# Performance work log

Hardware: AMD Instinct MI355X
Metric: run time of the kernel (lower is better)

Reference implementation:

```python
import jax, jax.numpy as jnp
import numpy as np

N_BINS = 229
OUT_F = 88
MODEL = 128
W_SIZE = 30
WIN = 2 * W_SIZE + 1  # 61


def _window(spec):
    B, T, F = spec.shape
    padded = jnp.pad(spec, ((0, 0), (W_SIZE, W_SIZE), (0, 0)))
    idx = jnp.arange(T)[:, None] + jnp.arange(WIN)[None, :]
    return padded[:, idx, :]


def setup_inputs() -> dict:
    key = jax.random.key(0)
    ks = jax.random.split(key, 12)
    B, T = 4, 1024
    s = 0.05
    return {
        "spec": jax.random.normal(ks[0], (B, T, N_BINS), dtype=jnp.float32),
        # frame_stack: Linear(N_BINS -> OUT_F)
        "W_frame": jax.random.normal(ks[1], (N_BINS, OUT_F), dtype=jnp.float32) * s,
        "b_frame": jnp.zeros((OUT_F,), dtype=jnp.float32),
        # onset attention: Linear(N_BINS + N_BINS -> MODEL), v: Linear(MODEL -> 1, no bias)
        "W_attn_o": jax.random.normal(ks[2], (2 * N_BINS, MODEL), dtype=jnp.float32) * s,
        "b_attn_o": jnp.zeros((MODEL,), dtype=jnp.float32),
        "v_o": jax.random.normal(ks[3], (MODEL,), dtype=jnp.float32) * s,
        # onset linear1: Linear(N_BINS -> OUT_F)
        "W_lin1": jax.random.normal(ks[4], (N_BINS, OUT_F), dtype=jnp.float32) * s,
        "b_lin1": jnp.zeros((OUT_F,), dtype=jnp.float32),
        # combine attention: Linear(2*OUT_F + N_BINS -> MODEL)
        "W_attn_c": jax.random.normal(ks[5], (2 * OUT_F + N_BINS, MODEL), dtype=jnp.float32) * s,
        "b_attn_c": jnp.zeros((MODEL,), dtype=jnp.float32),
        "v_c": jax.random.normal(ks[6], (MODEL,), dtype=jnp.float32) * s,
        # combine linear: Linear(2*OUT_F + N_BINS -> OUT_F)
        "W_linc": jax.random.normal(ks[7], (2 * OUT_F + N_BINS, OUT_F), dtype=jnp.float32) * s,
        "b_linc": jnp.zeros((OUT_F,), dtype=jnp.float32),
    }


def _attend(hidden, win, Wa, ba, v):
    B, T, Wn, F = win.shape
    h = jnp.broadcast_to(hidden[:, :, None, :], (B, T, Wn, hidden.shape[-1]))
    energy = jnp.tanh(jnp.concatenate([h, win], axis=-1) @ Wa + ba)
    scores = energy @ v
    return jax.nn.softmax(scores, axis=-1)


def reference(spec, W_frame, b_frame, W_attn_o, b_attn_o, v_o, W_lin1, b_lin1,
              W_attn_c, b_attn_c, v_c, W_linc, b_linc):
    win = _window(spec)

    feat_pred = spec @ W_frame + b_frame  # [B,T,OUT_F]

    # Onset stack
    a_onset = _attend(spec, win, W_attn_o, b_attn_o, v_o)
    weighted_o = jnp.einsum('btw,btwf->btf', a_onset, win)  # [B,T,N_BINS]
    onset_pred = jax.nn.sigmoid(weighted_o @ W_lin1 + b_lin1)  # [B,T,OUT_F]

    # Combine stack
    x = jnp.concatenate([feat_pred, onset_pred], axis=-1)  # [B,T,2*OUT_F]
    a_frame = _attend(x, win, W_attn_c, b_attn_c, v_c)
    weighted_c = jnp.einsum('btw,btwf->btf', a_frame, win)  # [B,T,N_BINS]
    frame_pred = jax.nn.sigmoid(jnp.concatenate([x, weighted_c], axis=-1) @ W_linc + b_linc)

    return (frame_pred, a_frame[:, :, None, :], onset_pred, a_onset[:, :, None, :], feat_pred)
```

## Files before the change

### kernel.cpp

```cpp
#include <hip/hip_runtime.h>

#define NBINS 229
#define OUTF  88
#define MODEL 128
#define WSZ   30
#define WIN   61
#define TLEN  1024
#define BT    4096

#define NC1 648
#define NP1 704
#define KP1 256
#define NC2 216
#define KP2 192

typedef short bf16x8 __attribute__((ext_vector_type(8)));
typedef float f32x4 __attribute__((ext_vector_type(4)));
typedef unsigned short ushort_t;

__device__ __forceinline__ float sigmoid_f(float x) {
    return __builtin_amdgcn_rcpf(1.f + __expf(-x));
}
__device__ __forceinline__ ushort_t f2bf(float f) {
    unsigned u = __float_as_uint(f);
    return (ushort_t)((u + 0x7fffu + ((u >> 16) & 1u)) >> 16);
}

#define PREP_BLOCKS 2181

__global__ __launch_bounds__(256) void prep_kernel(
    const float* __restrict__ Wf,  const float* __restrict__ bfr,
    const float* __restrict__ Wao, const float* __restrict__ bao,
    const float* __restrict__ Wl1,
    const float* __restrict__ Wac, const float* __restrict__ bac,
    const float* __restrict__ Wlc,
    const float* __restrict__ spec,
    const float* __restrict__ vo, const float* __restrict__ vc,
    ushort_t* __restrict__ B1b, ushort_t* __restrict__ B2b,
    ushort_t* __restrict__ specB, ushort_t* __restrict__ xB,
    float* __restrict__ bias1, float* __restrict__ bias2,
    float* __restrict__ sv)
{
    __shared__ float red[4];
    const int b = blockIdx.x;
    if (b < 704) {
        int idx = b * 256 + threadIdx.x;
        int n = idx >> 8, k = idx & 255;
        float v = 0.f;
        if (k < NBINS && n < NC1) {
            if (n < 88)       v = Wf[k * 88 + n];
            else if (n < 216) v = Wao[k * MODEL + (n - 88)];
            else if (n < 344) v = Wao[(k + NBINS) * MODEL + (n - 216)];
            else if (n < 472) v = Wac[(k + 176) * MODEL + (n - 344)];
            else if (n < 560) v = Wl1[k * 88 + (n - 472)];
            else              v = Wlc[(k + 176) * 88 + (n - 560)];
        }
        B1b[idx] = f2bf(v);
    } else if (b < 896) {
        int idx = (b - 704) * 256 + threadIdx.x;
        int n = idx / 192, k = idx - n * 192;
        float v = 0.f;
        if (k < 176 && n < NC2)
            v = (n < 128) ? Wac[k * MODEL + n] : Wlc[k * 88 + (n - 128)];
        B2b[idx] = f2bf(v);
    } else if (b < 1920) {
        int idx = (b - 896) * 256 + threadIdx.x;
        int r = idx >> 6, k4 = (idx & 63) * 4;
        const float* sp = spec + (size_t)r * NBINS;
        ushort4 o;
        o.x = (k4 + 0 < NBINS) ? f2bf(sp[k4 + 0]) : (ushort_t)0;
        o.y = (k4 + 1 < NBINS) ? f2bf(sp[k4 + 1]) : (ushort_t)0;
        o.z = (k4 + 2 < NBINS) ? f2bf(sp[k4 + 2]) : (ushort_t)0;
        o.w = (k4 + 3 < NBINS) ? f2bf(sp[k4 + 3]) : (ushort_t)0;
        *(ushort4*)&specB[(size_t)r * 256 + k4] = o;
    } else if (b < 2176) {
        int idx = (b - 1920) * 256 + threadIdx.x;
        int r = idx >> 4, c = 176 + (idx & 15);
        xB[(size_t)r * 192 + c] = 0;
    } else if (b < 2180) {
        int idx = (b - 2176) * 256 + threadIdx.x;
        if (idx < 704)
            bias1[idx] = (idx < 88) ? bfr[idx] : (idx < 216 ? bao[idx - 88] : 0.f);
        else if (idx < 960) {
            int n = idx - 704;
            bias2[n] = (n < 128) ? bac[n] : 0.f;
        }
    } else {
        int wid = threadIdx.x >> 6, lane = threadIdx.x & 63;
        const float* vp = (wid < 2) ? vo : vc;
        float val = vp[(wid & 1) * 64 + lane];
#pragma unroll
        for (int m = 32; m; m >>= 1) val += __shfl_xor(val, m, 64);
        if (lane == 0) red[wid] = val;
        __syncthreads();
        if (threadIdx.x == 0) {
            sv[0] = red[0] + red[1];
            sv[1] = red[2] + red[3];
        }
    }
}

template<int KITER, int RTS, int MODE>
__global__ __launch_bounds__(256) void gemm_mfma(
    const ushort_t* __restrict__ Ab, int lka,
    const ushort_t* __restrict__ Bb,
    const float* __restrict__ bias, int Nc,
    float* __restrict__ f0, ushort_t* __restrict__ u0,
    float* __restrict__ f1, ushort_t* __restrict__ u1,
    ushort_t* __restrict__ u2, ushort_t* __restrict__ u3,
    ushort_t* __restrict__ u4)
{
    const int tid = threadIdx.x;
    const int wv = tid >> 6, ln = tid & 63;
    const int l15 = ln & 15, qd = ln >> 4;
    const int flat = blockIdx.y * gridDim.x + blockIdx.x;
    const int e = flat & 7, kf = flat >> 3;
    const int rb = (e * (1 << RTS) + (kf & ((1 << RTS) - 1))) * 64;
    const int cb = (kf >> RTS) * 64;
    const int lkb = KITER * 32;

    const ushort_t* ap = Ab + (size_t)(rb + wv * 16 + l15) * lka + qd * 8;
    const ushort_t* bp[4];
#pragma unroll
    for (int nt = 0; nt < 4; nt++)
        bp[nt] = Bb + (size_t)(cb + nt * 16 + l15) * lkb + qd * 8;

    f32x4 acc[4];
#pragma unroll
    for (int nt = 0; nt < 4; nt++) acc[nt] = (f32x4){0.f, 0.f, 0.f, 0.f};

    bf16x8 af = *(const bf16x8*)ap, bfv[4];
#pragma unroll
    for (int nt = 0; nt < 4; nt++) bfv[nt] = *(const bf16x8*)bp[nt];

    for (int it = 0; it < KITER; it++) {
        bf16x8 an, bn[4];
        const int nk = (it + 1 < KITER) ? (it + 1) * 32 : 0;
        an = *(const bf16x8*)(ap + nk);
#pragma unroll
        for (int nt = 0; nt < 4; nt++) bn[nt] = *(const bf16x8*)(bp[nt] + nk);
#pragma unroll
        for (int nt = 0; nt < 4; nt++)
            acc[nt] = __builtin_amdgcn_mfma_f32_16x16x32_bf16(
                af, bfv[nt], acc[nt], 0, 0, 0);
        af = an;
#pragma unroll
        for (int nt = 0; nt < 4; nt++) bfv[nt] = bn[nt];
    }

    const int mbase = rb + wv * 16 + qd * 4;
#pragma unroll
    for (int nt = 0; nt < 4; nt++) {
        const int n = cb + nt * 16 + l15;
        if (n < Nc) {
            const float bn = bias[n];
#pragma unroll
            for (int r = 0; r < 4; r++) {
                const int m = mbase + r;
                float val = acc[nt][r] + bn;
                if (MODE == 0) {
                    if (n < 88) {
                        f0[(size_t)m * 88 + n] = val;
                        u0[(size_t)m * 192 + n] = f2bf(val);
                    } else if (n < 216) {
                        f1[(size_t)m * 128 + (n - 88)] = __expf(val + val);
                    } else if (n < 344) {
                        u1[(size_t)m * 128 + (n - 216)] = f2bf(__expf(val + val));
                    } else if (n < 472) {
                        u2[(size_t)m * 128 + (n - 344)] = f2bf(__expf(val + val));
                    } else if (n < 560) {
                        u3[(size_t)m * 96 + (n - 472)] = f2bf(val);
                    } else {
                        u4[(size_t)m * 96 + (n - 560)] = f2bf(val);
                    }
                } else {
                    f0[(size_t)m * 216 + n] = (n < 128) ? __expf(val + val) : val;
                }
            }
        }
    }
}

#define EPST 136
#define RST  96

__global__ __launch_bounds__(512) void attn_v8(
    const float* __restrict__ EH_all, int hs,
    const ushort_t* __restrict__ EPb,
    const ushort_t* __restrict__ Rb,
    const float* __restrict__ vvec, const float* __restrict__ svp,
    const float* __restrict__ pred_bias,
    const float* __restrict__ base, int bs,
    float* __restrict__ a_out, float* __restrict__ pred_out,
    ushort_t* __restrict__ xb)
{
    __shared__ ushort_t Pl[68 * EPST];
    __shared__ ushort_t Rl[68 * RST];

    const int tid = threadIdx.x;
    const int s0 = ((blockIdx.x & 7) * 64 + (blockIdx.x >> 3)) * 8;
    const int t0 = s0 & (TLEN - 1);

    for (int i = tid; i < 68 * 16; i += 512) {
        int j = i >> 4, c = (i & 15) * 8;
        int tg = t0 + j - WSZ;
        uint4 v = {0x3f803f80u, 0x3f803f80u, 0x3f803f80u, 0x3f803f80u};
        if ((unsigned)tg < (unsigned)TLEN)
            v = *(const uint4*)&EPb[(size_t)(s0 - WSZ + j) * 128 + c];
        *(uint4*)&Pl[j * EPST + c] = v;
    }
    for (int i = tid; i < 68 * 12; i += 512) {
        int j = i / 12, c = (i - j * 12) * 8;
        int tg = t0 + j - WSZ;
        uint4 v = {0u, 0u, 0u, 0u};
        if ((unsigned)tg < (unsigned)TLEN)
            v = *(const uint4*)&Rb[(size_t)(s0 - WSZ + j) * 96 + c];
        *(uint4*)&Rl[j * RST + c] = v;
    }
    __syncthreads();

    const int q = tid >> 6;
    const int w = tid & 63;
    const int s = s0 + q;
    const int su = __builtin_amdgcn_readfirstlane(s);
    const int row = q + ((w < WIN) ? w : 0);
    const ushort_t* pb = &Pl[row * EPST];
    const float* hrow = EH_all + (size_t)su * hs;
    const float sv = svp[0];

    float accr = 0.f;
#pragma unroll
    for (int d8 = 0; d8 < 16; d8++) {
        uint4 pv = *(const uint4*)(pb + d8 * 8);
        const float* hp = hrow + d8 * 8;
        const float* vp = vvec + d8 * 8;
        float p0 = __uint_as_float(pv.x << 16);
        float p1 = __uint_as_float(pv.x & 0xffff0000u);
        float p2 = __uint_as_float(pv.y << 16);
        float p3 = __uint_as_float(pv.y & 0xffff0000u);
        float p4 = __uint_as_float(pv.z << 16);
        float p5 = __uint_as_float(pv.z & 0xffff0000u);
        float p6 = __uint_as_float(pv.w << 16);
        float p7 = __uint_as_float(pv.w & 0xffff0000u);
        accr += vp[0] * __builtin_amdgcn_rcpf(__builtin_fmaf(hp[0], p0, 1.f));
        accr += vp[1] * __builtin_amdgcn_rcpf(__builtin_fmaf(hp[1], p1, 1.f));
        accr += vp[2] * __builtin_amdgcn_rcpf(__builtin_fmaf(hp[2], p2, 1.f));
        accr += vp[3] * __builtin_amdgcn_rcpf(__builtin_fmaf(hp[3], p3, 1.f));
        accr += vp[4] * __builtin_amdgcn_rcpf(__builtin_fmaf(hp[4], p4, 1.f));
        accr += vp[5] * __builtin_amdgcn_rcpf(__builtin_fmaf(hp[5], p5, 1.f));
        accr += vp[6] * __builtin_amdgcn_rcpf(__builtin_fmaf(hp[6], p6, 1.f));
        accr += vp[7] * __builtin_amdgcn_rcpf(__builtin_fmaf(hp[7], p7, 1.f));
    }
    float eng = sv - 2.f * accr;
    if (w >= WIN) eng = -1e30f;

    float mx = eng;
#pragma unroll
    for (int m = 32; m; m >>= 1) mx = fmaxf(mx, __shfl_xor(mx, m, 64));
    float ex = __expf(eng - mx);
    float sm = ex;
#pragma unroll
    for (int m = 32; m; m >>= 1) sm += __shfl_xor(sm, m, 64);
    float a = ex * __builtin_amdgcn_rcpf(sm);
    if (w < WIN) a_out[(size_t)s * WIN + w] = a;

    if (w < 44) {
        const int f = 2 * w;
        float acc0 = pred_bias[f], acc1 = pred_bias[f + 1];
        if (base) {
            acc0 += base[(size_t)s * bs + f];
            acc1 += base[(size_t)s * bs + f + 1];
        }
        const ushort_t* rr0 = &Rl[q * RST + f];
#pragma unroll
        for (int ww = 0; ww < WIN; ww++) {
            float aw = __uint_as_float(
                __builtin_amdgcn_readlane(__float_as_uint(a), ww));
            unsigned u = *(const unsigned*)(rr0 + ww * RST);
            acc0 += aw * __uint_as_float(u << 16);
            acc1 += aw * __uint_as_float(u & 0xffff0000u);
        }
        float p0 = sigmoid_f(acc0), p1 = sigmoid_f(acc1);
        *(float2*)&pred_out[(size_t)s * OUTF + f] = make_float2(p0, p1);
        if (xb) {
            ushort2 o; o.x = f2bf(p0); o.y = f2bf(p1);
            *(ushort2*)&xb[(size_t)s * 192 + 88 + f] = o;
        }
    }
}

extern "C" void kernel_launch(void* const* d_in, const int* in_sizes, int n_in,
                              void* d_out, int out_size, void* d_ws, size_t ws_size,
                              hipStream_t stream)
{
    const float* spec = (const float*)d_in[0];
    const float* Wf   = (const float*)d_in[1];
    const float* bf_  = (const float*)d_in[2];
    const float* Wao  = (const float*)d_in[3];
    const float* bao  = (const float*)d_in[4];
    const float* vo   = (const float*)d_in[5];
    const float* Wl1  = (const float*)d_in[6];
    const float* bl1  = (const float*)d_in[7];
    const float* Wac  = (const float*)d_in[8];
    const float* bac  = (const float*)d_in[9];
    const float* vc   = (const float*)d_in[10];
    const float* Wlc  = (const float*)d_in[11];
    const float* blc  = (const float*)d_in[12];

    float* out  = (float*)d_out;
    float* out0 = out;
    float* out1 = out + 360448;
    float* out2 = out + 610304;
    float* out3 = out + 970752;
    float* out4 = out + 1220608;

    float* ws = (float*)d_ws;
    float*    sv    = ws;
    float*    bias1 = ws + 16;
    float*    bias2 = ws + 720;
    ushort_t* B1b   = (ushort_t*)(ws + 976);
    ushort_t* B2b   = (ushort_t*)(ws + 91088);
    ushort_t* specB = (ushort_t*)(ws + 115664);
    ushort_t* xB    = (ushort_t*)(ws + 639952);
    float*    EHo   = ws + 1033168;
    ushort_t* EPo   = (ushort_t*)(ws + 1557456);
    ushort_t* EPc   = (ushort_t*)(ws + 1819600);
    ushort_t* Rb    = (ushort_t*)(ws + 2081744);
    ushort_t* Qb    = (ushort_t*)(ws + 2278352);
    float*    C2    = ws + 2474960;
    (void)ws_size; (void)in_sizes; (void)n_in; (void)out_size;

    prep_kernel<<<PREP_BLOCKS, 256, 0, stream>>>(
        Wf, bf_, Wao, bao, Wl1, Wac, bac, Wlc, spec, vo, vc,
        B1b, B2b, specB, xB, bias1, bias2, sv);

    gemm_mfma<8, 3, 0><<<dim3(NP1 / 64, 64), 256, 0, stream>>>(
        specB, 256, B1b, bias1, NC1, out4, xB, EHo, EPo, EPc, Rb, Qb);

    attn_v8<<<BT / 8, 512, 0, stream>>>(
        EHo, 128, EPo, Rb, vo, sv, bl1, nullptr, 0, out3, out2, xB);

    gemm_mfma<6, 3, 1><<<dim3(4, 64), 256, 0, stream>>>(
        xB, 192, B2b, bias2, NC2, C2, nullptr, nullptr, nullptr,
        nullptr, nullptr, nullptr);

    attn_v8<<<BT / 8, 512, 0, stream>>>(
        C2, 216, EPc, Qb, vc, sv + 1, blc, C2 + 128, 216, out1, out0, nullptr);
}
```

Measured before the change: 133.3 us.

## Split attention energy reduction across two waves per timestep

The attention kernel now handles 4 timesteps per block instead of 8, using two wavefronts per timestep. Each wave reduces half of the 128 model dimensions, and the partial sums are combined through shared memory after a barrier. The pred output columns are also split between the two waves. This doubles the grid and shortens each wave's serial dependency chain. In exchange it adds a block-wide barrier, duplicates the softmax work in both waves, and makes the shared-memory loads narrower (uint2 instead of uint4).

```diff
diff --git a/kernel.cpp b/kernel.cpp
--- a/kernel.cpp
+++ b/kernel.cpp
@@ -181,10 +181,10 @@
     }
 }
 
-#define EPST 136
+#define EPST 132
 #define RST  96
 
-__global__ __launch_bounds__(512) void attn_v8(
+__global__ __launch_bounds__(512) void attn_v9(
     const float* __restrict__ EH_all, int hs,
     const ushort_t* __restrict__ EPb,
     const ushort_t* __restrict__ Rb,
@@ -194,22 +194,23 @@
     float* __restrict__ a_out, float* __restrict__ pred_out,
     ushort_t* __restrict__ xb)
 {
-    __shared__ ushort_t Pl[68 * EPST];
-    __shared__ ushort_t Rl[68 * RST];
+    __shared__ ushort_t Pl[64 * EPST];
+    __shared__ ushort_t Rl[64 * RST];
+    __shared__ float Ep[4][2][64];
 
     const int tid = threadIdx.x;
-    const int s0 = ((blockIdx.x & 7) * 64 + (blockIdx.x >> 3)) * 8;
+    const int s0 = ((blockIdx.x & 7) * 128 + (blockIdx.x >> 3)) * 4;
     const int t0 = s0 & (TLEN - 1);
 
-    for (int i = tid; i < 68 * 16; i += 512) {
-        int j = i >> 4, c = (i & 15) * 8;
+    for (int i = tid; i < 64 * 32; i += 512) {
+        int j = i >> 5, c = (i & 31) * 4;
         int tg = t0 + j - WSZ;
-        uint4 v = {0x3f803f80u, 0x3f803f80u, 0x3f803f80u, 0x3f803f80u};
+        uint2 v = {0x3f803f80u, 0x3f803f80u};
         if ((unsigned)tg < (unsigned)TLEN)
-            v = *(const uint4*)&EPb[(size_t)(s0 - WSZ + j) * 128 + c];
-        *(uint4*)&Pl[j * EPST + c] = v;
-    }
-    for (int i = tid; i < 68 * 12; i += 512) {
+            v = *(const uint2*)&EPb[(size_t)(s0 - WSZ + j) * 128 + c];
+        *(uint2*)&Pl[j * EPST + c] = v;
+    }
+    for (int i = tid; i < 64 * 12; i += 512) {
         int j = i / 12, c = (i - j * 12) * 8;
         int tg = t0 + j - WSZ;
         uint4 v = {0u, 0u, 0u, 0u};
@@ -219,39 +220,36 @@
     }
     __syncthreads();
 
-    const int q = tid >> 6;
-    const int w = tid & 63;
-    const int s = s0 + q;
+    const int wv = tid >> 6;
+    const int q  = wv >> 1;
+    const int hf = wv & 1;
+    const int w  = tid & 63;
+    const int s  = s0 + q;
     const int su = __builtin_amdgcn_readfirstlane(s);
     const int row = q + ((w < WIN) ? w : 0);
-    const ushort_t* pb = &Pl[row * EPST];
-    const float* hrow = EH_all + (size_t)su * hs;
-    const float sv = svp[0];
+    const ushort_t* pb = &Pl[row * EPST + hf * 64];
+    const float* hrow = EH_all + (size_t)su * hs + hf * 64;
+    const float* vp0 = vvec + hf * 64;
 
     float accr = 0.f;
 #pragma unroll
-    for (int d8 = 0; d8 < 16; d8++) {
-        uint4 pv = *(const uint4*)(pb + d8 * 8);
-        const float* hp = hrow + d8 * 8;
-        const float* vp = vvec + d8 * 8;
+    for (int d4 = 0; d4 < 16; d4++) {
+        uint2 pv = *(const uint2*)(pb + d4 * 4);
+        const float* hp = hrow + d4 * 4;
+        const float* vp = vp0 + d4 * 4;
         float p0 = __uint_as_float(pv.x << 16);
         float p1 = __uint_as_float(pv.x & 0xffff0000u);
         float p2 = __uint_as_float(pv.y << 16);
         float p3 = __uint_as_float(pv.y & 0xffff0000u);
-        float p4 = __uint_as_float(pv.z << 16);
-        float p5 = __uint_as_float(pv.z & 0xffff0000u);
-        float p6 = __uint_as_float(pv.w << 16);
-        float p7 = __uint_as_float(pv.w & 0xffff0000u);
         accr += vp[0] * __builtin_amdgcn_rcpf(__builtin_fmaf(hp[0], p0, 1.f));
         accr += vp[1] * __builtin_amdgcn_rcpf(__builtin_fmaf(hp[1], p1, 1.f));
         accr += vp[2] * __builtin_amdgcn_rcpf(__builtin_fmaf(hp[2], p2, 1.f));
         accr += vp[3] * __builtin_amdgcn_rcpf(__builtin_fmaf(hp[3], p3, 1.f));
-        accr += vp[4] * __builtin_amdgcn_rcpf(__builtin_fmaf(hp[4], p4, 1.f));
-        accr += vp[5] * __builtin_amdgcn_rcpf(__builtin_fmaf(hp[5], p5, 1.f));
-        accr += vp[6] * __builtin_amdgcn_rcpf(__builtin_fmaf(hp[6], p6, 1.f));
-        accr += vp[7] * __builtin_amdgcn_rcpf(__builtin_fmaf(hp[7], p7, 1.f));
-    }
-    float eng = sv - 2.f * accr;
+    }
+    Ep[q][hf][w] = accr;
+    __syncthreads();
+
+    float eng = svp[0] - 2.f * (Ep[q][0][w] + Ep[q][1][w]);
     if (w >= WIN) eng = -1e30f;
 
     float mx = eng;
@@ -262,10 +260,10 @@
 #pragma unroll
     for (int m = 32; m; m >>= 1) sm += __shfl_xor(sm, m, 64);
     float a = ex * __builtin_amdgcn_rcpf(sm);
-    if (w < WIN) a_out[(size_t)s * WIN + w] = a;
-
-    if (w < 44) {
-        const int f = 2 * w;
+    if (hf == 0 && w < WIN) a_out[(size_t)s * WIN + w] = a;
+
+    if (w < 22) {
+        const int f = 44 * hf + 2 * w;
         float acc0 = pred_bias[f], acc1 = pred_bias[f + 1];
         if (base) {
             acc0 += base[(size_t)s * bs + f];
@@ -337,13 +335,13 @@
     gemm_mfma<8, 3, 0><<<dim3(NP1 / 64, 64), 256, 0, stream>>>(
         specB, 256, B1b, bias1, NC1, out4, xB, EHo, EPo, EPc, Rb, Qb);
 
-    attn_v8<<<BT / 8, 512, 0, stream>>>(
+    attn_v9<<<BT / 4, 512, 0, stream>>>(
         EHo, 128, EPo, Rb, vo, sv, bl1, nullptr, 0, out3, out2, xB);
 
     gemm_mfma<6, 3, 1><<<dim3(4, 64), 256, 0, stream>>>(
         xB, 192, B2b, bias2, NC2, C2, nullptr, nullptr, nullptr,
         nullptr, nullptr, nullptr);
 
-    attn_v8<<<BT / 8, 512, 0, stream>>>(
+    attn_v9<<<BT / 4, 512, 0, stream>>>(
         C2, 216, EPc, Qb, vc, sv + 1, blc, C2 + 128, 216, out1, out0, nullptr);
 }
```

After: 140.9 us. 5.7% more time.
